# Performance work log

Measured on AMD Instinct MI355X. Metric: run time of the kernel, lower is better.

The kernel has to match this reference:

```python
import jax, jax.numpy as jnp
import numpy as np

EPS = 1e-5  # torch.nn.CosineSimilarity eps


def setup_inputs() -> dict:
    key = jax.random.key(0)
    x = jax.random.normal(key, (8, 256, 1024), dtype=jnp.float32)
    return {"batch_sequence_tensors": x}


def _worst_sim(x):
    # For every contiguous window [s, e] (1 <= s < e <= S-1, matching
    # exclude_special_tokens + sequential combinatorics), compute
    # min_t in [s,e] cos(mean(x[s:e+1]), x[t]).
    # Trick: dot(sum_{s..e} x_i, x_t) comes from a prefix sum of the Gram
    # matrix, and ||sum_{s..e} x||^2 from a 2-D prefix sum of the Gram matrix,
    # avoiding any [B,S,S,D] intermediates.
    B, S, D = x.shape
    G = jnp.einsum('bsd,btd->bst', x, x)  # [B,S,S] Gram

    # num[b,s,e,t] = sum_{i=s..e} x_i . x_t  via 1-D prefix sum over i
    Cpad = jnp.pad(jnp.cumsum(G, axis=1), ((0, 0), (1, 0), (0, 0)))  # [B,S+1,S]
    num = Cpad[:, 1:, :][:, None, :, :] - Cpad[:, :S, :][:, :, None, :]  # [B,S,S,S]

    # ||sum_{s..e} x||^2 = sum_{i,j in [s,e]} G[i,j] via 2-D prefix sum
    PP = jnp.pad(jnp.cumsum(jnp.cumsum(G, axis=1), axis=2),
                 ((0, 0), (1, 0), (1, 0)))  # [B,S+1,S+1]
    dE = jnp.diagonal(PP[:, 1:, 1:], axis1=1, axis2=2)   # PP[e+1,e+1]  [B,S]
    dS = jnp.diagonal(PP[:, :S, :S], axis1=1, axis2=2)   # PP[s,s]      [B,S]
    cross1 = PP[:, :S, 1:]                               # PP[s,e+1]  axes (s,e)
    cross2 = jnp.swapaxes(PP[:, 1:, :S], 1, 2)           # PP[e+1,s] -> (s,e)
    ssq = dE[:, None, :] + dS[:, :, None] - cross1 - cross2  # [B,S,S]
    sum_norm = jnp.sqrt(jnp.maximum(ssq, 0.0))               # ||sum||

    idx = jnp.arange(S)
    win_len = jnp.maximum(idx[None, :] - idx[:, None] + 1, 1).astype(x.dtype)  # [S,S] (s,e)
    # center = sum / len ; cosine uses the mean exactly as the torch module
    mean_norm = sum_norm / win_len                       # [B,S,S]
    x_norm = jnp.sqrt(jnp.maximum(jnp.diagonal(G, axis1=1, axis2=2), 0.0))  # [B,S]
    denom = jnp.maximum(mean_norm[..., None] * x_norm[:, None, None, :], EPS)
    cos = (num / win_len[None, :, :, None]) / denom      # [B,S,S,S]

    t_in = (idx[None, None, :] >= idx[:, None, None]) & \
           (idx[None, None, :] <= idx[None, :, None])    # [S,S,S] (s,e,t)
    worst = jnp.min(jnp.where(t_in[None], cos, jnp.inf), axis=-1)  # [B,S,S]

    valid = (idx[:, None] >= 1) & (idx[None, :] > idx[:, None])    # 1<=s<e<=S-1
    return jnp.where(valid[None], worst, 0.0)


def reference(batch_sequence_tensors):
    # worst_sim[b,s,e] = min cosine similarity of window mean vs members;
    # the original module's group mask is worst_sim >= threshold (0.9),
    # followed by (data-dependent, non-tensor) subset removal.
    return _worst_sim(batch_sequence_tensors)
```

## Files before the change

### kernel.cpp

```cpp
#include <hip/hip_runtime.h>
#include <stdint.h>

#define NB 8
#define NS 256
#define ND 1024
#define EPSF 1e-5f
#define BIGF 3.0e38f

typedef __attribute__((ext_vector_type(8))) short short8;
typedef __attribute__((ext_vector_type(4))) float f32x4;

__device__ __forceinline__ unsigned short f2bf(float f) {
  unsigned int u = __float_as_uint(f);
  u = (u + 0x7FFFu + ((u >> 16) & 1u)) >> 16;
  return (unsigned short)u;
}

__global__ __launch_bounds__(256) void k_pre(const float* __restrict__ x,
                                             unsigned short* __restrict__ Xb,
                                             unsigned short* __restrict__ Yb,
                                             float* __restrict__ DGa,
                                             float* __restrict__ IXa) {
  __shared__ struct { float xt[256][9]; float tot[8][33]; } sm;
  int blk = blockIdx.x;
  int tid = threadIdx.x;
  int lane = tid & 63;

  if (blk < 512) {
    int row = blk * 4 + (tid >> 6);
    size_t base = (size_t)row * ND;
    float sq = 0.f;
#pragma unroll
    for (int c = 0; c < 4; ++c) {
      size_t o = base + c * 256 + lane * 4;
      float4 v = *reinterpret_cast<const float4*>(x + o);
      ushort4 ob;
      ob.x = f2bf(v.x); ob.y = f2bf(v.y); ob.z = f2bf(v.z); ob.w = f2bf(v.w);
      *reinterpret_cast<ushort4*>(Xb + o) = ob;
      sq += v.x * v.x + v.y * v.y + v.z * v.z + v.w * v.w;
    }
#pragma unroll
    for (int off = 32; off; off >>= 1) sq += __shfl_xor(sq, off);
    if (lane == 0) {
      DGa[row] = sq;
      IXa[row] = 1.0f / sqrtf(sq);
    }
    return;
  }

  int tile = blk - 512;
  int b = tile >> 7;
  int d0 = (tile & 127) << 3;
  const float* xs = x + ((size_t)b << 18) + d0;
#pragma unroll
  for (int q = 0; q < 2; ++q) {
    int slot = tid + (q << 8);
    int s = slot >> 1, h = (slot & 1) << 2;
    float4 v = *reinterpret_cast<const float4*>(xs + (size_t)s * ND + h);
    sm.xt[s][h + 0] = v.x;
    sm.xt[s][h + 1] = v.y;
    sm.xt[s][h + 2] = v.z;
    sm.xt[s][h + 3] = v.w;
  }
  __syncthreads();
  int col = tid & 7, ch = tid >> 3;
  float loc[8];
  float run = 0.f;
#pragma unroll
  for (int r = 0; r < 8; ++r) { run += sm.xt[ch * 8 + r][col]; loc[r] = run; }
  sm.tot[col][ch] = run;
  __syncthreads();
#pragma unroll
  for (int off = 1; off < 32; off <<= 1) {
    float tv = (ch >= off) ? sm.tot[col][ch - off] : 0.f;
    __syncthreads();
    sm.tot[col][ch] += tv;
    __syncthreads();
  }
  float excl = sm.tot[col][ch] - run;
#pragma unroll
  for (int r = 0; r < 8; ++r) sm.xt[ch * 8 + r][col] = excl + loc[r];
  __syncthreads();
  unsigned short* yr = Yb + ((size_t)b << 18) + (size_t)tid * ND + d0;
  ushort4 o0, o1;
  o0.x = f2bf(sm.xt[tid][0]); o0.y = f2bf(sm.xt[tid][1]);
  o0.z = f2bf(sm.xt[tid][2]); o0.w = f2bf(sm.xt[tid][3]);
  o1.x = f2bf(sm.xt[tid][4]); o1.y = f2bf(sm.xt[tid][5]);
  o1.z = f2bf(sm.xt[tid][6]); o1.w = f2bf(sm.xt[tid][7]);
  reinterpret_cast<ushort4*>(yr)[0] = o0;
  reinterpret_cast<ushort4*>(yr)[1] = o1;
}

__global__ __launch_bounds__(256) void k_gemmC(const unsigned short* __restrict__ yb,
                                               const unsigned short* __restrict__ xb,
                                               float* __restrict__ C) {
  int job = (blockIdx.x << 2) + (threadIdx.x >> 6);
  int lane = threadIdx.x & 63;
  int b = job >> 8;
  int mt = (job >> 4) & 15;
  int nt = job & 15;
  const unsigned short* Ab = yb + ((size_t)b << 18) + ((size_t)(mt << 4) << 10);
  const unsigned short* Bb = xb + ((size_t)b << 18) + ((size_t)(nt << 4) << 10);
  int lr = lane & 15;
  int kbase = (lane >> 4) << 3;
  f32x4 ae = {0.f, 0.f, 0.f, 0.f}, ao = {0.f, 0.f, 0.f, 0.f};
#pragma unroll 4
  for (int kk = 0; kk < 1024; kk += 64) {
    const unsigned short* ap = Ab + ((size_t)lr << 10) + kbase + kk;
    const unsigned short* bp = Bb + ((size_t)lr << 10) + kbase + kk;
    short8 a0 = *reinterpret_cast<const short8*>(ap);
    short8 b0 = *reinterpret_cast<const short8*>(bp);
    short8 a1 = *reinterpret_cast<const short8*>(ap + 32);
    short8 b1 = *reinterpret_cast<const short8*>(bp + 32);
    ae = __builtin_amdgcn_mfma_f32_16x16x32_bf16(a0, b0, ae, 0, 0, 0);
    ao = __builtin_amdgcn_mfma_f32_16x16x32_bf16(a1, b1, ao, 0, 0, 0);
  }
  f32x4 acc = ae + ao;
  float* Cb = C + (size_t)b * 257 * NS;
  int r0 = (mt << 4) + ((lane >> 4) << 2) + 1;
  int c0 = (nt << 4) + lr;
#pragma unroll
  for (int j = 0; j < 4; ++j) Cb[(size_t)(r0 + j) * NS + c0] = acc[j];
}

__global__ __launch_bounds__(256) void k_scan(float* __restrict__ C, float* __restrict__ S2) {
  int id = blockIdx.x * 4 + (threadIdx.x >> 6);
  int lane = threadIdx.x & 63;
  int b = id / 257;
  int r = id - b * 257;
  float* Crow = C + ((size_t)b * 257 + r) * NS;
  float* Srow = S2 + ((size_t)b * 257 + r) * 257;
  if (lane == 0) Srow[0] = 0.f;
  float run = 0.f;
  for (int c0 = 0; c0 < NS; c0 += 64) {
    float v;
    if (r > 0) {
      v = Crow[c0 + lane];
    } else {
      v = 0.f;
      Crow[c0 + lane] = 0.f;
    }
#pragma unroll
    for (int off = 1; off < 64; off <<= 1) {
      float n = __shfl_up(v, off);
      if (lane >= off) v += n;
    }
    Srow[c0 + lane + 1] = run + v;
    run += __shfl(v, 63);
  }
}

__global__ __launch_bounds__(256) void k_trop(const float* __restrict__ C,
                                              const float* __restrict__ S2,
                                              const float* __restrict__ IXa,
                                              const float* __restrict__ DGa,
                                              float* __restrict__ out) {
  __shared__ float As[64][36];
  __shared__ float Bs[64][68];
  __shared__ float wred[4];
  int blk = blockIdx.x;
  int b = blk >> 5;
  int tix = blk & 31;
  int i0 = (tix >> 2) << 5;
  int j0 = (tix & 3) << 6;
  int tid = threadIdx.x;
  float* outb = out + ((size_t)b << 16);

  if (i0 >= j0 + 63) {
    float4 z = {0.f, 0.f, 0.f, 0.f};
    float* p = outb + (size_t)(i0 + (tid >> 3)) * NS + j0 + ((tid & 7) << 3);
    reinterpret_cast<float4*>(p)[0] = z;
    reinterpret_cast<float4*>(p)[1] = z;
    return;
  }

  const float* Cb = C + (size_t)b * 257 * NS;
  const float* IXb = IXa + b * NS;

  float wv0 = IXb[tid];
#pragma unroll
  for (int off = 32; off; off >>= 1) wv0 = fmaxf(wv0, __shfl_xor(wv0, off));
  if ((tid & 63) == 0) wred[tid >> 6] = wv0;
  __syncthreads();
  float wmb = fmaxf(fmaxf(wred[0], wred[1]), fmaxf(wred[2], wred[3]));

  int ii0 = (tid >> 4) << 1;
  int jj0 = (tid & 15) << 2;
  float acc[8];
#pragma unroll
  for (int k = 0; k < 8; ++k) acc[k] = BIGF;

  int rA = tid >> 4;
  int c4 = (tid & 15) << 2;

  for (int t0 = i0 & ~63; t0 < j0 + 64; t0 += 64) {
    __syncthreads();
    float4 wv = *reinterpret_cast<const float4*>(IXb + t0 + c4);
#pragma unroll
    for (int p = 0; p < 2; ++p) {
      int r = i0 + p * 16 + rA;
      float4 v = *reinterpret_cast<const float4*>(Cb + (size_t)r * NS + t0 + c4);
      As[c4 + 0][p * 16 + rA] = v.x * wv.x;
      As[c4 + 1][p * 16 + rA] = v.y * wv.y;
      As[c4 + 2][p * 16 + rA] = v.z * wv.z;
      As[c4 + 3][p * 16 + rA] = v.w * wv.w;
    }
#pragma unroll
    for (int p = 0; p < 4; ++p) {
      int r = j0 + 1 + p * 16 + rA;
      float4 v = *reinterpret_cast<const float4*>(Cb + (size_t)r * NS + t0 + c4);
      Bs[c4 + 0][p * 16 + rA] = v.x * wv.x;
      Bs[c4 + 1][p * 16 + rA] = v.y * wv.y;
      Bs[c4 + 2][p * 16 + rA] = v.z * wv.z;
      Bs[c4 + 3][p * 16 + rA] = v.w * wv.w;
    }
    __syncthreads();

    int thA = i0 + ii0 - t0;
    int thB = j0 + jj0 - t0;
    if (thA <= -1 && thB >= 63) {
#pragma unroll 4
      for (int tt = 0; tt < 64; ++tt) {
        float2 a = *reinterpret_cast<const float2*>(&As[tt][ii0]);
        float4 bv = *reinterpret_cast<const float4*>(&Bs[tt][jj0]);
        acc[0] = fminf(acc[0], bv.x - a.x);
        acc[1] = fminf(acc[1], bv.y - a.x);
        acc[2] = fminf(acc[2], bv.z - a.x);
        acc[3] = fminf(acc[3], bv.w - a.x);
        acc[4] = fminf(acc[4], bv.x - a.y);
        acc[5] = fminf(acc[5], bv.y - a.y);
        acc[6] = fminf(acc[6], bv.z - a.y);
        acc[7] = fminf(acc[7], bv.w - a.y);
      }
    } else {
#pragma unroll 4
      for (int tt = 0; tt < 64; ++tt) {
        float2 a = *reinterpret_cast<const float2*>(&As[tt][ii0]);
        float4 bv = *reinterpret_cast<const float4*>(&Bs[tt][jj0]);
        float a0 = (tt >= thA)     ? a.x  : -BIGF;
        float a1 = (tt >= thA + 1) ? a.y  : -BIGF;
        float b0 = (tt <= thB)     ? bv.x :  BIGF;
        float b1 = (tt <= thB + 1) ? bv.y :  BIGF;
        float b2 = (tt <= thB + 2) ? bv.z :  BIGF;
        float b3 = (tt <= thB + 3) ? bv.w :  BIGF;
        acc[0] = fminf(acc[0], b0 - a0);
        acc[1] = fminf(acc[1], b1 - a0);
        acc[2] = fminf(acc[2], b2 - a0);
        acc[3] = fminf(acc[3], b3 - a0);
        acc[4] = fminf(acc[4], b0 - a1);
        acc[5] = fminf(acc[5], b1 - a1);
        acc[6] = fminf(acc[6], b2 - a1);
        acc[7] = fminf(acc[7], b3 - a1);
      }
    }
  }

  const float* S2b = S2 + (size_t)b * 257 * 257;
  const float* DGb = DGa + b * NS;
#pragma unroll
  for (int k = 0; k < 2; ++k) {
    int i = i0 + ii0 + k;
    float o4[4];
    float s2ii = S2b[(size_t)i * 257 + i];
#pragma unroll
    for (int l = 0; l < 4; ++l) {
      int j = j0 + jj0 + l;
      float res = 0.f;
      if (i >= 1 && j > i) {
        float s2jj = S2b[(size_t)(j + 1) * 257 + (j + 1)];
        float s2ij = S2b[(size_t)i * 257 + (j + 1)];
        float s2ji = S2b[(size_t)(j + 1) * 257 + i];
        float ssq = (s2jj - s2ij) - (s2ji - s2ii);
        float sn = sqrtf(fmaxf(ssq, 0.f));
        float win = (float)(j - i + 1);
        if (sn >= EPSF * win * wmb) {
          res = acc[k * 4 + l] / sn;
        } else {
          float mn = sn / win;
          float m = BIGF;
          const float* r2 = Cb + (size_t)(j + 1) * NS;
          const float* r1 = Cb + (size_t)i * NS;
          for (int t = i; t <= j; ++t) {
            float num = r2[t] - r1[t];
            float xn = sqrtf(fmaxf(DGb[t], 0.f));
            float den = fmaxf(mn * xn, EPSF);
            m = fminf(m, num / win / den);
          }
          res = m;
        }
      }
      o4[l] = res;
    }
    float4 st = {o4[0], o4[1], o4[2], o4[3]};
    *reinterpret_cast<float4*>(outb + (size_t)i * NS + j0 + jj0) = st;
  }
}

extern "C" void kernel_launch(void* const* d_in, const int* in_sizes, int n_in,
                              void* d_out, int out_size, void* d_ws, size_t ws_size,
                              hipStream_t stream) {
  (void)in_sizes; (void)n_in; (void)ws_size; (void)out_size;
  const float* x = (const float*)d_in[0];
  float* out = (float*)d_out;
  char* ws = (char*)d_ws;
  unsigned short* Xb = (unsigned short*)(ws);
  unsigned short* Yb = (unsigned short*)(ws + 4194304);
  float* C   = (float*)(ws + 8388608);
  float* S2  = (float*)(ws + 10493952);
  float* DGa = (float*)(ws + 12607520);
  float* IXa = (float*)(ws + 12615712);

  k_pre<<<1536, 256, 0, stream>>>(x, Xb, Yb, DGa, IXa);
  k_gemmC<<<512, 256, 0, stream>>>(Yb, Xb, C);
  k_scan<<<514, 256, 0, stream>>>(C, S2);
  k_trop<<<256, 256, 0, stream>>>(C, S2, IXa, DGa, out);
}
```

Measured before the change: 109.1 us.

## Fuse prefix-scan into tropical kernel, computing window norms in shared memory

Removes the separate k_scan kernel and S2 buffer; each k_trop block recomputes the row prefix sums it needs for its i-rows and j-rows and assembles the squared window norms in a shared tile. This eliminates one launch and the global write/read of the 2-D prefix-sum array. In exchange, blocks redo scans over overlapping rows and the kernel no longer zeroes C row 0.

```diff
diff --git a/kernel.cpp b/kernel.cpp
--- a/kernel.cpp
+++ b/kernel.cpp
@@ -123,40 +123,13 @@
   for (int j = 0; j < 4; ++j) Cb[(size_t)(r0 + j) * NS + c0] = acc[j];
 }
 
-__global__ __launch_bounds__(256) void k_scan(float* __restrict__ C, float* __restrict__ S2) {
-  int id = blockIdx.x * 4 + (threadIdx.x >> 6);
-  int lane = threadIdx.x & 63;
-  int b = id / 257;
-  int r = id - b * 257;
-  float* Crow = C + ((size_t)b * 257 + r) * NS;
-  float* Srow = S2 + ((size_t)b * 257 + r) * 257;
-  if (lane == 0) Srow[0] = 0.f;
-  float run = 0.f;
-  for (int c0 = 0; c0 < NS; c0 += 64) {
-    float v;
-    if (r > 0) {
-      v = Crow[c0 + lane];
-    } else {
-      v = 0.f;
-      Crow[c0 + lane] = 0.f;
-    }
-#pragma unroll
-    for (int off = 1; off < 64; off <<= 1) {
-      float n = __shfl_up(v, off);
-      if (lane >= off) v += n;
-    }
-    Srow[c0 + lane + 1] = run + v;
-    run += __shfl(v, 63);
-  }
-}
-
 __global__ __launch_bounds__(256) void k_trop(const float* __restrict__ C,
-                                              const float* __restrict__ S2,
                                               const float* __restrict__ IXa,
                                               const float* __restrict__ DGa,
                                               float* __restrict__ out) {
   __shared__ float As[64][36];
   __shared__ float Bs[64][68];
+  __shared__ float ssq_t[32][65];
   __shared__ float wred[4];
   int blk = blockIdx.x;
   int b = blk >> 5;
@@ -164,6 +137,8 @@
   int i0 = (tix >> 2) << 5;
   int j0 = (tix & 3) << 6;
   int tid = threadIdx.x;
+  int wv = tid >> 6;
+  int lane = tid & 63;
   float* outb = out + ((size_t)b << 16);
 
   if (i0 >= j0 + 63) {
@@ -177,10 +152,55 @@
   const float* Cb = C + (size_t)b * 257 * NS;
   const float* IXb = IXa + b * NS;
 
+  for (int rr = 0; rr < 8; ++rr) {
+    int r = i0 + (wv << 3) + rr;
+    const float* Crow = Cb + (size_t)r * NS;
+    float carry = 0.f, pii = 0.f;
+    int ii = r - i0;
+    for (int c0 = 0; c0 < NS; c0 += 64) {
+      float v = Crow[c0 + lane];
+      float s = v;
+#pragma unroll
+      for (int off = 1; off < 64; off <<= 1) {
+        float n = __shfl_up(s, off);
+        if (lane >= off) s += n;
+      }
+      float excl = carry + s - v;
+      if (c0 == (r & ~63)) pii = __shfl(excl, r & 63);
+      int c = c0 + lane;
+      if (c >= j0 + 1 && c <= j0 + 64) ssq_t[ii][c - j0 - 1] = pii - excl;
+      carry += __shfl(s, 63);
+    }
+    if (j0 == 192 && lane == 0) ssq_t[ii][63] = pii - carry;
+  }
+  __syncthreads();
+  for (int rr = 0; rr < 16; ++rr) {
+    int jr = j0 + 1 + (wv << 4) + rr;
+    int jl = jr - 1 - j0;
+    const float* Crow = Cb + (size_t)jr * NS;
+    float carry = 0.f, pd = 0.f, pji = 0.f;
+    for (int c0 = 0; c0 < NS; c0 += 64) {
+      float v = Crow[c0 + lane];
+      float s = v;
+#pragma unroll
+      for (int off = 1; off < 64; off <<= 1) {
+        float n = __shfl_up(s, off);
+        if (lane >= off) s += n;
+      }
+      float excl = carry + s - v;
+      if (c0 == (i0 & ~63)) pji = __shfl(excl, (i0 & 63) + (lane & 31));
+      if (jr < 256 && c0 == (jr & ~63)) pd = __shfl(excl, jr & 63);
+      carry += __shfl(s, 63);
+    }
+    if (jr == 256) pd = carry;
+    if (lane < 32) ssq_t[lane][jl] += pd - pji;
+  }
+  __syncthreads();
+
   float wv0 = IXb[tid];
 #pragma unroll
   for (int off = 32; off; off >>= 1) wv0 = fmaxf(wv0, __shfl_xor(wv0, off));
-  if ((tid & 63) == 0) wred[tid >> 6] = wv0;
+  if (lane == 0) wred[wv] = wv0;
   __syncthreads();
   float wmb = fmaxf(fmaxf(wred[0], wred[1]), fmaxf(wred[2], wred[3]));
 
@@ -195,24 +215,24 @@
 
   for (int t0 = i0 & ~63; t0 < j0 + 64; t0 += 64) {
     __syncthreads();
-    float4 wv = *reinterpret_cast<const float4*>(IXb + t0 + c4);
+    float4 wvx = *reinterpret_cast<const float4*>(IXb + t0 + c4);
 #pragma unroll
     for (int p = 0; p < 2; ++p) {
       int r = i0 + p * 16 + rA;
       float4 v = *reinterpret_cast<const float4*>(Cb + (size_t)r * NS + t0 + c4);
-      As[c4 + 0][p * 16 + rA] = v.x * wv.x;
-      As[c4 + 1][p * 16 + rA] = v.y * wv.y;
-      As[c4 + 2][p * 16 + rA] = v.z * wv.z;
-      As[c4 + 3][p * 16 + rA] = v.w * wv.w;
+      As[c4 + 0][p * 16 + rA] = v.x * wvx.x;
+      As[c4 + 1][p * 16 + rA] = v.y * wvx.y;
+      As[c4 + 2][p * 16 + rA] = v.z * wvx.z;
+      As[c4 + 3][p * 16 + rA] = v.w * wvx.w;
     }
 #pragma unroll
     for (int p = 0; p < 4; ++p) {
       int r = j0 + 1 + p * 16 + rA;
       float4 v = *reinterpret_cast<const float4*>(Cb + (size_t)r * NS + t0 + c4);
-      Bs[c4 + 0][p * 16 + rA] = v.x * wv.x;
-      Bs[c4 + 1][p * 16 + rA] = v.y * wv.y;
-      Bs[c4 + 2][p * 16 + rA] = v.z * wv.z;
-      Bs[c4 + 3][p * 16 + rA] = v.w * wv.w;
+      Bs[c4 + 0][p * 16 + rA] = v.x * wvx.x;
+      Bs[c4 + 1][p * 16 + rA] = v.y * wvx.y;
+      Bs[c4 + 2][p * 16 + rA] = v.z * wvx.z;
+      Bs[c4 + 3][p * 16 + rA] = v.w * wvx.w;
     }
     __syncthreads();
 
@@ -255,22 +275,17 @@
     }
   }
 
-  const float* S2b = S2 + (size_t)b * 257 * 257;
   const float* DGb = DGa + b * NS;
 #pragma unroll
   for (int k = 0; k < 2; ++k) {
     int i = i0 + ii0 + k;
     float o4[4];
-    float s2ii = S2b[(size_t)i * 257 + i];
 #pragma unroll
     for (int l = 0; l < 4; ++l) {
       int j = j0 + jj0 + l;
       float res = 0.f;
       if (i >= 1 && j > i) {
-        float s2jj = S2b[(size_t)(j + 1) * 257 + (j + 1)];
-        float s2ij = S2b[(size_t)i * 257 + (j + 1)];
-        float s2ji = S2b[(size_t)(j + 1) * 257 + i];
-        float ssq = (s2jj - s2ij) - (s2ji - s2ii);
+        float ssq = ssq_t[ii0 + k][jj0 + l];
         float sn = sqrtf(fmaxf(ssq, 0.f));
         float win = (float)(j - i + 1);
         if (sn >= EPSF * win * wmb) {
@@ -306,12 +321,10 @@
   unsigned short* Xb = (unsigned short*)(ws);
   unsigned short* Yb = (unsigned short*)(ws + 4194304);
   float* C   = (float*)(ws + 8388608);
-  float* S2  = (float*)(ws + 10493952);
-  float* DGa = (float*)(ws + 12607520);
-  float* IXa = (float*)(ws + 12615712);
+  float* DGa = (float*)(ws + 10493952);
+  float* IXa = (float*)(ws + 10502144);
 
   k_pre<<<1536, 256, 0, stream>>>(x, Xb, Yb, DGa, IXa);
   k_gemmC<<<512, 256, 0, stream>>>(Yb, Xb, C);
-  k_scan<<<514, 256, 0, stream>>>(C, S2);
-  k_trop<<<256, 256, 0, stream>>>(C, S2, IXa, DGa, out);
-}
+  k_trop<<<256, 256, 0, stream>>>(C, IXa, DGa, out);
+}
```

Result: slower. 148.6 us (+36.1%).

## Fuse window norm computation into tropical kernel and drop the scan kernel

Applied to the files above, without the earlier changes.

Removes the separate row prefix-scan kernel and its 2-D prefix-sum buffer. The squared norm of each window sum is now accumulated inside the tropical min loop, as the sum over t of the same differences used for the cosine numerators. Because the raw differences are needed for that sum, the per-t inverse-norm weight is no longer folded into shared-memory staging. It is applied with a multiply in the inner loop instead, so the inner loop roughly doubles its ALU work in exchange for one fewer launch and less memory traffic. The zeroing of C row 0 that the scan used to do is gone, so correctness depends on that row being zeroed elsewhere.

```diff
diff --git a/kernel.cpp b/kernel.cpp
--- a/kernel.cpp
+++ b/kernel.cpp
@@ -123,40 +123,13 @@
   for (int j = 0; j < 4; ++j) Cb[(size_t)(r0 + j) * NS + c0] = acc[j];
 }
 
-__global__ __launch_bounds__(256) void k_scan(float* __restrict__ C, float* __restrict__ S2) {
-  int id = blockIdx.x * 4 + (threadIdx.x >> 6);
-  int lane = threadIdx.x & 63;
-  int b = id / 257;
-  int r = id - b * 257;
-  float* Crow = C + ((size_t)b * 257 + r) * NS;
-  float* Srow = S2 + ((size_t)b * 257 + r) * 257;
-  if (lane == 0) Srow[0] = 0.f;
-  float run = 0.f;
-  for (int c0 = 0; c0 < NS; c0 += 64) {
-    float v;
-    if (r > 0) {
-      v = Crow[c0 + lane];
-    } else {
-      v = 0.f;
-      Crow[c0 + lane] = 0.f;
-    }
-#pragma unroll
-    for (int off = 1; off < 64; off <<= 1) {
-      float n = __shfl_up(v, off);
-      if (lane >= off) v += n;
-    }
-    Srow[c0 + lane + 1] = run + v;
-    run += __shfl(v, 63);
-  }
-}
-
 __global__ __launch_bounds__(256) void k_trop(const float* __restrict__ C,
-                                              const float* __restrict__ S2,
                                               const float* __restrict__ IXa,
                                               const float* __restrict__ DGa,
                                               float* __restrict__ out) {
   __shared__ float As[64][36];
   __shared__ float Bs[64][68];
+  __shared__ float wls[64];
   __shared__ float wred[4];
   int blk = blockIdx.x;
   int b = blk >> 5;
@@ -164,6 +137,8 @@
   int i0 = (tix >> 2) << 5;
   int j0 = (tix & 3) << 6;
   int tid = threadIdx.x;
+  int wv = tid >> 6;
+  int lane = tid & 63;
   float* outb = out + ((size_t)b << 16);
 
   if (i0 >= j0 + 63) {
@@ -180,39 +155,45 @@
   float wv0 = IXb[tid];
 #pragma unroll
   for (int off = 32; off; off >>= 1) wv0 = fmaxf(wv0, __shfl_xor(wv0, off));
-  if ((tid & 63) == 0) wred[tid >> 6] = wv0;
+  if (lane == 0) wred[wv] = wv0;
   __syncthreads();
   float wmb = fmaxf(fmaxf(wred[0], wred[1]), fmaxf(wred[2], wred[3]));
 
   int ii0 = (tid >> 4) << 1;
   int jj0 = (tid & 15) << 2;
-  float acc[8];
-#pragma unroll
-  for (int k = 0; k < 8; ++k) acc[k] = BIGF;
+  float acc[8], sq[8];
+#pragma unroll
+  for (int k = 0; k < 8; ++k) { acc[k] = BIGF; sq[k] = 0.f; }
 
   int rA = tid >> 4;
   int c4 = (tid & 15) << 2;
 
   for (int t0 = i0 & ~63; t0 < j0 + 64; t0 += 64) {
     __syncthreads();
-    float4 wv = *reinterpret_cast<const float4*>(IXb + t0 + c4);
+    if (tid < 16) {
+      float4 w = *reinterpret_cast<const float4*>(IXb + t0 + (tid << 2));
+      wls[(tid << 2) + 0] = w.x;
+      wls[(tid << 2) + 1] = w.y;
+      wls[(tid << 2) + 2] = w.z;
+      wls[(tid << 2) + 3] = w.w;
+    }
 #pragma unroll
     for (int p = 0; p < 2; ++p) {
       int r = i0 + p * 16 + rA;
       float4 v = *reinterpret_cast<const float4*>(Cb + (size_t)r * NS + t0 + c4);
-      As[c4 + 0][p * 16 + rA] = v.x * wv.x;
-      As[c4 + 1][p * 16 + rA] = v.y * wv.y;
-      As[c4 + 2][p * 16 + rA] = v.z * wv.z;
-      As[c4 + 3][p * 16 + rA] = v.w * wv.w;
+      As[c4 + 0][p * 16 + rA] = v.x;
+      As[c4 + 1][p * 16 + rA] = v.y;
+      As[c4 + 2][p * 16 + rA] = v.z;
+      As[c4 + 3][p * 16 + rA] = v.w;
     }
 #pragma unroll
     for (int p = 0; p < 4; ++p) {
       int r = j0 + 1 + p * 16 + rA;
       float4 v = *reinterpret_cast<const float4*>(Cb + (size_t)r * NS + t0 + c4);
-      Bs[c4 + 0][p * 16 + rA] = v.x * wv.x;
-      Bs[c4 + 1][p * 16 + rA] = v.y * wv.y;
-      Bs[c4 + 2][p * 16 + rA] = v.z * wv.z;
-      Bs[c4 + 3][p * 16 + rA] = v.w * wv.w;
+      Bs[c4 + 0][p * 16 + rA] = v.x;
+      Bs[c4 + 1][p * 16 + rA] = v.y;
+      Bs[c4 + 2][p * 16 + rA] = v.z;
+      Bs[c4 + 3][p * 16 + rA] = v.w;
     }
     __syncthreads();
 
@@ -221,56 +202,53 @@
     if (thA <= -1 && thB >= 63) {
 #pragma unroll 4
       for (int tt = 0; tt < 64; ++tt) {
+        float wt = wls[tt];
         float2 a = *reinterpret_cast<const float2*>(&As[tt][ii0]);
         float4 bv = *reinterpret_cast<const float4*>(&Bs[tt][jj0]);
-        acc[0] = fminf(acc[0], bv.x - a.x);
-        acc[1] = fminf(acc[1], bv.y - a.x);
-        acc[2] = fminf(acc[2], bv.z - a.x);
-        acc[3] = fminf(acc[3], bv.w - a.x);
-        acc[4] = fminf(acc[4], bv.x - a.y);
-        acc[5] = fminf(acc[5], bv.y - a.y);
-        acc[6] = fminf(acc[6], bv.z - a.y);
-        acc[7] = fminf(acc[7], bv.w - a.y);
+        float d0 = bv.x - a.x, d1 = bv.y - a.x, d2 = bv.z - a.x, d3 = bv.w - a.x;
+        float d4 = bv.x - a.y, d5 = bv.y - a.y, d6 = bv.z - a.y, d7 = bv.w - a.y;
+        acc[0] = fminf(acc[0], d0 * wt); sq[0] += d0;
+        acc[1] = fminf(acc[1], d1 * wt); sq[1] += d1;
+        acc[2] = fminf(acc[2], d2 * wt); sq[2] += d2;
+        acc[3] = fminf(acc[3], d3 * wt); sq[3] += d3;
+        acc[4] = fminf(acc[4], d4 * wt); sq[4] += d4;
+        acc[5] = fminf(acc[5], d5 * wt); sq[5] += d5;
+        acc[6] = fminf(acc[6], d6 * wt); sq[6] += d6;
+        acc[7] = fminf(acc[7], d7 * wt); sq[7] += d7;
       }
     } else {
 #pragma unroll 4
       for (int tt = 0; tt < 64; ++tt) {
+        float wt = wls[tt];
         float2 a = *reinterpret_cast<const float2*>(&As[tt][ii0]);
         float4 bv = *reinterpret_cast<const float4*>(&Bs[tt][jj0]);
-        float a0 = (tt >= thA)     ? a.x  : -BIGF;
-        float a1 = (tt >= thA + 1) ? a.y  : -BIGF;
-        float b0 = (tt <= thB)     ? bv.x :  BIGF;
-        float b1 = (tt <= thB + 1) ? bv.y :  BIGF;
-        float b2 = (tt <= thB + 2) ? bv.z :  BIGF;
-        float b3 = (tt <= thB + 3) ? bv.w :  BIGF;
-        acc[0] = fminf(acc[0], b0 - a0);
-        acc[1] = fminf(acc[1], b1 - a0);
-        acc[2] = fminf(acc[2], b2 - a0);
-        acc[3] = fminf(acc[3], b3 - a0);
-        acc[4] = fminf(acc[4], b0 - a1);
-        acc[5] = fminf(acc[5], b1 - a1);
-        acc[6] = fminf(acc[6], b2 - a1);
-        acc[7] = fminf(acc[7], b3 - a1);
+        bool va0 = tt >= thA, va1 = tt >= thA + 1;
+        bool vb0 = tt <= thB, vb1 = tt <= thB + 1, vb2 = tt <= thB + 2, vb3 = tt <= thB + 3;
+        float d0 = bv.x - a.x, d1 = bv.y - a.x, d2 = bv.z - a.x, d3 = bv.w - a.x;
+        float d4 = bv.x - a.y, d5 = bv.y - a.y, d6 = bv.z - a.y, d7 = bv.w - a.y;
+        acc[0] = fminf(acc[0], (va0 && vb0) ? d0 * wt : BIGF); sq[0] += (va0 && vb0) ? d0 : 0.f;
+        acc[1] = fminf(acc[1], (va0 && vb1) ? d1 * wt : BIGF); sq[1] += (va0 && vb1) ? d1 : 0.f;
+        acc[2] = fminf(acc[2], (va0 && vb2) ? d2 * wt : BIGF); sq[2] += (va0 && vb2) ? d2 : 0.f;
+        acc[3] = fminf(acc[3], (va0 && vb3) ? d3 * wt : BIGF); sq[3] += (va0 && vb3) ? d3 : 0.f;
+        acc[4] = fminf(acc[4], (va1 && vb0) ? d4 * wt : BIGF); sq[4] += (va1 && vb0) ? d4 : 0.f;
+        acc[5] = fminf(acc[5], (va1 && vb1) ? d5 * wt : BIGF); sq[5] += (va1 && vb1) ? d5 : 0.f;
+        acc[6] = fminf(acc[6], (va1 && vb2) ? d6 * wt : BIGF); sq[6] += (va1 && vb2) ? d6 : 0.f;
+        acc[7] = fminf(acc[7], (va1 && vb3) ? d7 * wt : BIGF); sq[7] += (va1 && vb3) ? d7 : 0.f;
       }
     }
   }
 
-  const float* S2b = S2 + (size_t)b * 257 * 257;
   const float* DGb = DGa + b * NS;
 #pragma unroll
   for (int k = 0; k < 2; ++k) {
     int i = i0 + ii0 + k;
     float o4[4];
-    float s2ii = S2b[(size_t)i * 257 + i];
 #pragma unroll
     for (int l = 0; l < 4; ++l) {
       int j = j0 + jj0 + l;
       float res = 0.f;
       if (i >= 1 && j > i) {
-        float s2jj = S2b[(size_t)(j + 1) * 257 + (j + 1)];
-        float s2ij = S2b[(size_t)i * 257 + (j + 1)];
-        float s2ji = S2b[(size_t)(j + 1) * 257 + i];
-        float ssq = (s2jj - s2ij) - (s2ji - s2ii);
+        float ssq = sq[k * 4 + l];
         float sn = sqrtf(fmaxf(ssq, 0.f));
         float win = (float)(j - i + 1);
         if (sn >= EPSF * win * wmb) {
@@ -306,12 +284,10 @@
   unsigned short* Xb = (unsigned short*)(ws);
   unsigned short* Yb = (unsigned short*)(ws + 4194304);
   float* C   = (float*)(ws + 8388608);
-  float* S2  = (float*)(ws + 10493952);
-  float* DGa = (float*)(ws + 12607520);
-  float* IXa = (float*)(ws + 12615712);
+  float* DGa = (float*)(ws + 10493952);
+  float* IXa = (float*)(ws + 10502144);
 
   k_pre<<<1536, 256, 0, stream>>>(x, Xb, Yb, DGa, IXa);
   k_gemmC<<<512, 256, 0, stream>>>(Yb, Xb, C);
-  k_scan<<<514, 256, 0, stream>>>(C, S2);
-  k_trop<<<256, 256, 0, stream>>>(C, S2, IXa, DGa, out);
-}
+  k_trop<<<256, 256, 0, stream>>>(C, IXa, DGa, out);
+}
```

New measurement: 110.9 us. No clear change (+1.6%).
